# Kernel tuning notes

Measured on AMD Instinct MI355X. Metric: run time of the kernel, lower is better.

The kernel has to match this reference:

```python
import jax, jax.numpy as jnp
import numpy as np

N_NODES = 150000
N_EDGES = 4800000
IN_DIM, HID_DIM, OUT_DIM = 1433, 16, 7


def setup_inputs() -> dict:
    key = jax.random.key(0)
    ks = jax.random.split(key, 8)
    features = jax.random.normal(ks[0], (N_NODES, IN_DIM), dtype=jnp.float32)
    edge_src = jax.random.randint(ks[1], (N_EDGES,), 0, N_NODES, dtype=jnp.int32)
    edge_dst = jax.random.randint(ks[2], (N_EDGES,), 0, N_NODES, dtype=jnp.int32)
    adj_vals = jax.random.uniform(ks[3], (N_EDGES,), dtype=jnp.float32)
    W1 = jax.random.normal(ks[4], (IN_DIM, HID_DIM), dtype=jnp.float32) * (1.0 / np.sqrt(IN_DIM))
    b1 = jnp.zeros((HID_DIM,), dtype=jnp.float32)
    W2 = jax.random.normal(ks[5], (HID_DIM, OUT_DIM), dtype=jnp.float32) * (1.0 / np.sqrt(HID_DIM))
    b2 = jnp.zeros((OUT_DIM,), dtype=jnp.float32)
    return {"features": features, "edge_src": edge_src, "edge_dst": edge_dst,
            "adj_vals": adj_vals, "W1": W1, "b1": b1, "W2": W2, "b2": b2}


def _gcn_layer(x, edge_src, edge_dst, adj_vals, W, b):
    # h = A_hat @ (x @ W) + b ; dense transform first since in_dim >= out_dim
    xw = x @ W                                   # [N, d_out]
    msg = adj_vals[:, None] * xw[edge_src]       # [E, d_out] gather
    agg = jax.ops.segment_sum(msg, edge_dst, num_segments=x.shape[0])  # scatter-add
    return agg + b


def reference(features, edge_src, edge_dst, adj_vals, W1, b1, W2, b2):
    h1 = jax.nn.relu(_gcn_layer(features, edge_src, edge_dst, adj_vals, W1, b1))
    # dropout in original forward is a no-op (result discarded) -> omitted
    h2 = _gcn_layer(h1, edge_src, edge_dst, adj_vals, W2, b2)
    return jax.nn.log_softmax(h2, axis=1)
```

## Files before the change

### kernel.cpp

```cpp
#include <hip/hip_runtime.h>
#include <float.h>
#include <stdint.h>

#define IN_DIM 1433
#define HID 16
#define OUTD 7

#define KC 32
#define GROWS 64
#define NT 45
#define KLAST 25

#define AS1 __attribute__((address_space(1)))
#define AS3 __attribute__((address_space(3)))

__global__ __launch_bounds__(256, 4) void gemm1_kernel(
    const float* __restrict__ feat, const float* __restrict__ W1,
    float* __restrict__ xw1, int N)
{
    __shared__ float xs[3][GROWS * KC];
    const int t = threadIdx.x;
    const int lane = t & 63;
    const int w = t >> 6;
    const int row0 = blockIdx.x * GROWS;
    const long maxElem = (long)N * IN_DIM - 1;

    const int r  = t & 63;
    const int rb = r & 7;
    const int q4 = __builtin_amdgcn_readfirstlane(w) * 4;

    long ebase[8];
#pragma unroll
    for (int i = 0; i < 8; ++i) {
        const int ri = (i * 4 + w) * 2 + (lane >> 5);
        const int cs = lane & 31;
        const int gcol = (cs & 3) | (((cs >> 2) ^ (ri & 7)) << 2);
        ebase[i] = (long)(row0 + ri) * IN_DIM + gcol;
    }

    float acc[4] = {0.f, 0.f, 0.f, 0.f};

    auto stage = [&](int buf, int k0) {
#pragma unroll
        for (int i = 0; i < 8; ++i) {
            long elem = ebase[i] + k0;
            if (elem > maxElem) elem = maxElem;
            __builtin_amdgcn_global_load_lds(
                (const AS1 void*)(feat + elem),
                (AS3 void*)(&xs[buf][(i * 4 + w) * 64]), 4, 0, 0);
        }
    };

#define COMPUTE(buf, k0v, KMAX)                                              \
    {                                                                        \
        const float* xrow = &xs[buf][r * KC];                                \
        _Pragma("unroll")                                                    \
        for (int b = 0; b < ((KMAX) >> 2); ++b) {                            \
            const float4 xv = *(const float4*)&xrow[((b ^ rb) << 2)];        \
            const float* wk = W1 + (size_t)((k0v) + 4 * b) * HID + q4;       \
            const float4 w0 = *(const float4*)(wk);                          \
            const float4 w1 = *(const float4*)(wk + HID);                    \
            const float4 w2 = *(const float4*)(wk + 2 * HID);                \
            const float4 w3 = *(const float4*)(wk + 3 * HID);                \
            acc[0] += xv.x * w0.x; acc[1] += xv.x * w0.y;                    \
            acc[2] += xv.x * w0.z; acc[3] += xv.x * w0.w;                    \
            acc[0] += xv.y * w1.x; acc[1] += xv.y * w1.y;                    \
            acc[2] += xv.y * w1.z; acc[3] += xv.y * w1.w;                    \
            acc[0] += xv.z * w2.x; acc[1] += xv.z * w2.y;                    \
            acc[2] += xv.z * w2.z; acc[3] += xv.z * w2.w;                    \
            acc[0] += xv.w * w3.x; acc[1] += xv.w * w3.y;                    \
            acc[2] += xv.w * w3.z; acc[3] += xv.w * w3.w;                    \
        }                                                                    \
        if ((KMAX) & 3) {                     \
            const int b = (KMAX) >> 2;                                       \
            const float4 xv = *(const float4*)&xrow[((b ^ rb) << 2)];        \
            const float* wk = W1 + (size_t)((k0v) + 4 * b) * HID + q4;       \
            const float4 w0 = *(const float4*)(wk);                          \
            acc[0] += xv.x * w0.x; acc[1] += xv.x * w0.y;                    \
            acc[2] += xv.x * w0.z; acc[3] += xv.x * w0.w;                    \
        }                                                                    \
    }

#define WAITBAR(Nimm)                                                        \
    asm volatile("s_waitcnt vmcnt(" #Nimm ")" ::: "memory");                 \
    __builtin_amdgcn_sched_barrier(0);                                       \
    __builtin_amdgcn_s_barrier();                                            \
    __builtin_amdgcn_sched_barrier(0);

    stage(0, 0);
    stage(1, KC);
    for (int g = 0; g < 13; ++g) {
        const int k0 = g * (3 * KC);
        WAITBAR(8); stage(2, k0 + 2 * KC); COMPUTE(0, k0, KC);
        WAITBAR(8); stage(0, k0 + 3 * KC); COMPUTE(1, k0 + KC, KC);
        WAITBAR(8); stage(1, k0 + 4 * KC); COMPUTE(2, k0 + 2 * KC, KC);
    }
    WAITBAR(8); stage(2, 41 * KC); COMPUTE(0, 39 * KC, KC);
    WAITBAR(8); stage(0, 42 * KC); COMPUTE(1, 40 * KC, KC);
    WAITBAR(8); stage(1, 43 * KC); COMPUTE(2, 41 * KC, KC);
    WAITBAR(8); stage(2, 44 * KC); COMPUTE(0, 42 * KC, KC);
    WAITBAR(8);                    COMPUTE(1, 43 * KC, KC);
    WAITBAR(0);                    COMPUTE(2, 44 * KC, KLAST);
#undef COMPUTE
#undef WAITBAR

    const int grow = row0 + r;
    if (grow < N)
        *(float4*)(xw1 + (size_t)grow * HID + q4) =
            make_float4(acc[0], acc[1], acc[2], acc[3]);
}

__global__ __launch_bounds__(256) void hist_kernel(
    const int* __restrict__ dst, int* __restrict__ cnt, int E)
{
    const int e = blockIdx.x * 256 + threadIdx.x;
    if (e < E) atomicAdd(&cnt[dst[e]], 1);
}

__global__ __launch_bounds__(256) void scan1_kernel(
    const int* __restrict__ cnt, int* __restrict__ offs,
    int* __restrict__ bsum, int N)
{
    __shared__ int lds[256];
    const int t = threadIdx.x, b = blockIdx.x;
    const int base = b * 1024 + t * 4;
    int c0 = 0, c1 = 0, c2 = 0, c3 = 0;
    if (base + 0 < N) c0 = cnt[base + 0];
    if (base + 1 < N) c1 = cnt[base + 1];
    if (base + 2 < N) c2 = cnt[base + 2];
    if (base + 3 < N) c3 = cnt[base + 3];
    const int s = c0 + c1 + c2 + c3;
    lds[t] = s;
    __syncthreads();
    for (int off = 1; off < 256; off <<= 1) {
        int v = (t >= off) ? lds[t - off] : 0;
        __syncthreads();
        lds[t] += v;
        __syncthreads();
    }
    const int excl = lds[t] - s;
    if (t == 255) bsum[b] = lds[255];
    int run = excl;
    if (base + 0 < N) { offs[base + 0] = run; run += c0; }
    if (base + 1 < N) { offs[base + 1] = run; run += c1; }
    if (base + 2 < N) { offs[base + 2] = run; run += c2; }
    if (base + 3 < N) { offs[base + 3] = run; run += c3; }
}

__global__ __launch_bounds__(256) void scan2_kernel(
    const int* __restrict__ bsum, int* __restrict__ bbase, int NB)
{
    __shared__ int lds[256];
    const int t = threadIdx.x;
    const int v = (t < NB) ? bsum[t] : 0;
    lds[t] = v;
    __syncthreads();
    for (int off = 1; off < 256; off <<= 1) {
        int u = (t >= off) ? lds[t - off] : 0;
        __syncthreads();
        lds[t] += u;
        __syncthreads();
    }
    bbase[t] = lds[t] - v;
}

__global__ __launch_bounds__(256) void scan3_kernel(
    int* __restrict__ offs, int* __restrict__ cursor,
    const int* __restrict__ bbase, int N, int E)
{
    const int t = threadIdx.x, b = blockIdx.x;
    const int add = bbase[b];
    const int base = b * 1024 + t * 4;
#pragma unroll
    for (int i = 0; i < 4; ++i) {
        const int idx = base + i;
        if (idx < N) {
            const int v = offs[idx] + add;
            offs[idx] = v;
            cursor[idx] = v;
        }
    }
    if (b == 0 && t == 0) offs[N] = E;
}

__global__ __launch_bounds__(256) void fill_kernel(
    const int* __restrict__ src, const int* __restrict__ dst,
    const float* __restrict__ a, int* __restrict__ cursor,
    uint2* __restrict__ pairs, int E)
{
    const int e = blockIdx.x * 256 + threadIdx.x;
    if (e >= E) return;
    const int d = dst[e];
    const int pos = atomicAdd(&cursor[d], 1);
    pairs[pos] = make_uint2((unsigned)src[e], __float_as_uint(a[e]));
}

__global__ __launch_bounds__(256) void gather1_kernel(
    const uint2* __restrict__ pairs, const int* __restrict__ offs,
    const float* __restrict__ xw1, const float* __restrict__ b1,
    const float* __restrict__ W2, float* __restrict__ xw2, int N)
{
    __shared__ float w2s[HID * OUTD];
    const int t = threadIdx.x;
    if (t < HID * OUTD) w2s[t] = W2[t];
    __syncthreads();
    const int lane = t & 63;
    const int r = blockIdx.x * 4 + (t >> 6);
    if (r >= N) return;
    const int g = lane >> 2;
    const int c = lane & 3;
    const int start = offs[r], end = offs[r + 1];
    float4 acc = make_float4(0.f, 0.f, 0.f, 0.f);
    int e = start + g;
    for (; e + 16 < end; e += 32) {
        const uint2 p0 = pairs[e];
        const uint2 p1 = pairs[e + 16];
        const float4 v0 = *(const float4*)(xw1 + (size_t)p0.x * HID + c * 4);
        const float4 v1 = *(const float4*)(xw1 + (size_t)p1.x * HID + c * 4);
        const float a0 = __uint_as_float(p0.y);
        const float a1 = __uint_as_float(p1.y);
        acc.x += a0 * v0.x + a1 * v1.x;
        acc.y += a0 * v0.y + a1 * v1.y;
        acc.z += a0 * v0.z + a1 * v1.z;
        acc.w += a0 * v0.w + a1 * v1.w;
    }
    if (e < end) {
        const uint2 p0 = pairs[e];
        const float4 v0 = *(const float4*)(xw1 + (size_t)p0.x * HID + c * 4);
        const float a0 = __uint_as_float(p0.y);
        acc.x += a0 * v0.x; acc.y += a0 * v0.y;
        acc.z += a0 * v0.z; acc.w += a0 * v0.w;
    }
#pragma unroll
    for (int m = 4; m < 64; m <<= 1) {
        acc.x += __shfl_xor(acc.x, m);
        acc.y += __shfl_xor(acc.y, m);
        acc.z += __shfl_xor(acc.z, m);
        acc.w += __shfl_xor(acc.w, m);
    }
    const float4 b1v = ((const float4*)b1)[c];
    float4 hv;
    hv.x = fmaxf(acc.x + b1v.x, 0.f);
    hv.y = fmaxf(acc.y + b1v.y, 0.f);
    hv.z = fmaxf(acc.z + b1v.z, 0.f);
    hv.w = fmaxf(acc.w + b1v.w, 0.f);
    float hh[16];
#pragma unroll
    for (int cc = 0; cc < 4; ++cc) {
        hh[cc * 4 + 0] = __shfl(hv.x, cc);
        hh[cc * 4 + 1] = __shfl(hv.y, cc);
        hh[cc * 4 + 2] = __shfl(hv.z, cc);
        hh[cc * 4 + 3] = __shfl(hv.w, cc);
    }
    const int col = (lane & 7) < OUTD ? (lane & 7) : 0;
    float sacc = 0.f;
#pragma unroll
    for (int j = 0; j < HID; ++j) sacc += hh[j] * w2s[j * OUTD + col];
    if (lane < 8) xw2[(size_t)r * 8 + lane] = (lane < OUTD) ? sacc : 0.f;
}

__global__ __launch_bounds__(256) void gather2_kernel(
    const uint2* __restrict__ pairs, const int* __restrict__ offs,
    const float* __restrict__ xw2, const float* __restrict__ b2,
    float* __restrict__ out, int N)
{
    const int t = threadIdx.x;
    const int lane = t & 63;
    const int r = blockIdx.x * 4 + (t >> 6);
    if (r >= N) return;
    const int g = lane >> 1;
    const int c = lane & 1;
    const int start = offs[r], end = offs[r + 1];
    float4 acc = make_float4(0.f, 0.f, 0.f, 0.f);
    for (int e = start + g; e < end; e += 32) {
        const uint2 p = pairs[e];
        const float4 v = *(const float4*)(xw2 + (size_t)p.x * 8 + c * 4);
        const float a = __uint_as_float(p.y);
        acc.x += a * v.x; acc.y += a * v.y;
        acc.z += a * v.z; acc.w += a * v.w;
    }
#pragma unroll
    for (int m = 2; m < 64; m <<= 1) {
        acc.x += __shfl_xor(acc.x, m);
        acc.y += __shfl_xor(acc.y, m);
        acc.z += __shfl_xor(acc.z, m);
        acc.w += __shfl_xor(acc.w, m);
    }
    float4 x;
    if (c == 0) {
        const float4 b2v = *(const float4*)b2;
        x.x = acc.x + b2v.x; x.y = acc.y + b2v.y;
        x.z = acc.z + b2v.z; x.w = acc.w + b2v.w;
    } else {
        x.x = acc.x + b2[4]; x.y = acc.y + b2[5];
        x.z = acc.z + b2[6]; x.w = -FLT_MAX;
    }
    float mymax = fmaxf(fmaxf(x.x, x.y), x.z);
    if (c == 0) mymax = fmaxf(mymax, x.w);
    const float m = fmaxf(mymax, __shfl_xor(mymax, 1));
    float es = expf(x.x - m) + expf(x.y - m) + expf(x.z - m);
    if (c == 0) es += expf(x.w - m);
    const float s = es + __shfl_xor(es, 1);
    const float lg = logf(s);
    float* op = out + (size_t)r * OUTD;
    if (c == 0) {
        op[0] = x.x - m - lg; op[1] = x.y - m - lg;
        op[2] = x.z - m - lg; op[3] = x.w - m - lg;
    } else {
        op[4] = x.x - m - lg; op[5] = x.y - m - lg;
        op[6] = x.z - m - lg;
    }
}

extern "C" void kernel_launch(void* const* d_in, const int* in_sizes, int n_in,
                              void* d_out, int out_size, void* d_ws, size_t ws_size,
                              hipStream_t stream)
{
    const float* feat  = (const float*)d_in[0];
    const int*   esrc  = (const int*)d_in[1];
    const int*   edst  = (const int*)d_in[2];
    const float* avals = (const float*)d_in[3];
    const float* W1    = (const float*)d_in[4];
    const float* b1    = (const float*)d_in[5];
    const float* W2    = (const float*)d_in[6];
    const float* b2    = (const float*)d_in[7];
    float* out = (float*)d_out;

    const int N = in_sizes[0] / IN_DIM;
    const int E = in_sizes[1];
    const int NB = (N + 1023) / 1024;

    char* p = (char*)d_ws;
    float* xw1   = (float*)p; p += (size_t)N * HID * sizeof(float);
    float* xw2   = (float*)p; p += (size_t)N * 8 * sizeof(float);
    int*   cnt   = (int*)p;   p += (size_t)N * sizeof(int);
    int*   offs  = (int*)p;   p += (size_t)(N + 1) * sizeof(int);
    int*   cursor= (int*)p;   p += (size_t)N * sizeof(int);
    int*   bsum  = (int*)p;   p += 256 * sizeof(int);
    int*   bbase = (int*)p;   p += 256 * sizeof(int);
    p = (char*)(((uintptr_t)p + 15) & ~(uintptr_t)15);
    uint2* pairs = (uint2*)p;

    hipMemsetAsync(cnt, 0, (size_t)N * sizeof(int), stream);

    gemm1_kernel<<<(N + GROWS - 1) / GROWS, 256, 0, stream>>>(feat, W1, xw1, N);

    hist_kernel<<<(E + 255) / 256, 256, 0, stream>>>(edst, cnt, E);
    scan1_kernel<<<NB, 256, 0, stream>>>(cnt, offs, bsum, N);
    scan2_kernel<<<1, 256, 0, stream>>>(bsum, bbase, NB);
    scan3_kernel<<<NB, 256, 0, stream>>>(offs, cursor, bbase, N, E);
    fill_kernel<<<(E + 255) / 256, 256, 0, stream>>>(esrc, edst, avals, cursor, pairs, E);

    gather1_kernel<<<(N + 3) / 4, 256, 0, stream>>>(pairs, offs, xw1, b1, W2, xw2, N);
    gather2_kernel<<<(N + 3) / 4, 256, 0, stream>>>(pairs, offs, xw2, b2, out, N);
}
```

Baseline: 1.181 ms.

## Make GEMM1 wave-independent: each wave owns 64 rows and all 16 outputs

Restructures the feature GEMM so that each wavefront stages its own 64 rows into private LDS buffers and computes all 16 hidden outputs per row. Before, four waves shared the tile and each computed a 4-column slice. The triple-buffered pipeline with block-wide s_barrier becomes double buffering with only vmcnt waits, which removes inter-wave synchronisation. The cost is 16 accumulators per thread, 32 async loads per stage per wave and smaller 128-thread blocks, which raises register pressure and changes occupancy.

```diff
diff --git a/kernel.cpp b/kernel.cpp
--- a/kernel.cpp
+++ b/kernel.cpp
@@ -7,107 +7,117 @@
 #define OUTD 7
 
 #define KC 32
-#define GROWS 64
 #define NT 45
-#define KLAST 25
 
 #define AS1 __attribute__((address_space(1)))
 #define AS3 __attribute__((address_space(3)))
 
-__global__ __launch_bounds__(256, 4) void gemm1_kernel(
+__global__ __launch_bounds__(128, 2) void gemm1_kernel(
     const float* __restrict__ feat, const float* __restrict__ W1,
     float* __restrict__ xw1, int N)
 {
-    __shared__ float xs[3][GROWS * KC];
+    __shared__ float xs[2][2][64 * KC];
     const int t = threadIdx.x;
     const int lane = t & 63;
     const int w = t >> 6;
-    const int row0 = blockIdx.x * GROWS;
+    const int row0 = blockIdx.x * 128 + w * 64;
+    const int l5 = lane >> 5;
+    const int cs = lane & 31;
     const long maxElem = (long)N * IN_DIM - 1;
 
-    const int r  = t & 63;
-    const int rb = r & 7;
-    const int q4 = __builtin_amdgcn_readfirstlane(w) * 4;
-
-    long ebase[8];
-#pragma unroll
-    for (int i = 0; i < 8; ++i) {
-        const int ri = (i * 4 + w) * 2 + (lane >> 5);
-        const int cs = lane & 31;
-        const int gcol = (cs & 3) | (((cs >> 2) ^ (ri & 7)) << 2);
-        ebase[i] = (long)(row0 + ri) * IN_DIM + gcol;
-    }
-
-    float acc[4] = {0.f, 0.f, 0.f, 0.f};
+    int co[4];
+#pragma unroll
+    for (int m = 0; m < 4; ++m)
+        co[m] = (cs & 3) | (((cs >> 2) ^ ((2 * m + l5) & 7)) << 2);
+
+    const long A = (long)(row0 + l5) * IN_DIM;
 
     auto stage = [&](int buf, int k0) {
 #pragma unroll
-        for (int i = 0; i < 8; ++i) {
-            long elem = ebase[i] + k0;
+        for (int i = 0; i < 32; ++i) {
+            long elem = A + (long)(2 * i) * IN_DIM + k0 + co[i & 3];
             if (elem > maxElem) elem = maxElem;
             __builtin_amdgcn_global_load_lds(
                 (const AS1 void*)(feat + elem),
-                (AS3 void*)(&xs[buf][(i * 4 + w) * 64]), 4, 0, 0);
+                (AS3 void*)(&xs[w][buf][(2 * i) * KC]), 4, 0, 0);
         }
     };
 
-#define COMPUTE(buf, k0v, KMAX)                                              \
+    const int r  = lane;
+    const int rb = r & 7;
+    float acc[16];
+#pragma unroll
+    for (int j = 0; j < 16; ++j) acc[j] = 0.f;
+
+#define COMPUTE(buf, k0v, NB4, TAIL)                                         \
     {                                                                        \
-        const float* xrow = &xs[buf][r * KC];                                \
+        const float* xrow = &xs[w][buf][r * KC];                             \
         _Pragma("unroll")                                                    \
-        for (int b = 0; b < ((KMAX) >> 2); ++b) {                            \
+        for (int b = 0; b < (NB4); ++b) {                                    \
             const float4 xv = *(const float4*)&xrow[((b ^ rb) << 2)];        \
-            const float* wk = W1 + (size_t)((k0v) + 4 * b) * HID + q4;       \
-            const float4 w0 = *(const float4*)(wk);                          \
-            const float4 w1 = *(const float4*)(wk + HID);                    \
-            const float4 w2 = *(const float4*)(wk + 2 * HID);                \
-            const float4 w3 = *(const float4*)(wk + 3 * HID);                \
-            acc[0] += xv.x * w0.x; acc[1] += xv.x * w0.y;                    \
-            acc[2] += xv.x * w0.z; acc[3] += xv.x * w0.w;                    \
-            acc[0] += xv.y * w1.x; acc[1] += xv.y * w1.y;                    \
-            acc[2] += xv.y * w1.z; acc[3] += xv.y * w1.w;                    \
-            acc[0] += xv.z * w2.x; acc[1] += xv.z * w2.y;                    \
-            acc[2] += xv.z * w2.z; acc[3] += xv.z * w2.w;                    \
-            acc[0] += xv.w * w3.x; acc[1] += xv.w * w3.y;                    \
-            acc[2] += xv.w * w3.z; acc[3] += xv.w * w3.w;                    \
+            const float* wk = W1 + (size_t)((k0v) + 4 * b) * HID;            \
+            _Pragma("unroll")                                                \
+            for (int e = 0; e < 4; ++e) {                                    \
+                const float xe = ((const float*)&xv)[e];                     \
+                const float4 wA = *(const float4*)(wk + e * HID);            \
+                const float4 wB = *(const float4*)(wk + e * HID + 4);        \
+                const float4 wC = *(const float4*)(wk + e * HID + 8);        \
+                const float4 wD = *(const float4*)(wk + e * HID + 12);       \
+                acc[0]  += xe * wA.x; acc[1]  += xe * wA.y;                  \
+                acc[2]  += xe * wA.z; acc[3]  += xe * wA.w;                  \
+                acc[4]  += xe * wB.x; acc[5]  += xe * wB.y;                  \
+                acc[6]  += xe * wB.z; acc[7]  += xe * wB.w;                  \
+                acc[8]  += xe * wC.x; acc[9]  += xe * wC.y;                  \
+                acc[10] += xe * wC.z; acc[11] += xe * wC.w;                  \
+                acc[12] += xe * wD.x; acc[13] += xe * wD.y;                  \
+                acc[14] += xe * wD.z; acc[15] += xe * wD.w;                  \
+            }                                                                \
         }                                                                    \
-        if ((KMAX) & 3) {                     \
-            const int b = (KMAX) >> 2;                                       \
-            const float4 xv = *(const float4*)&xrow[((b ^ rb) << 2)];        \
-            const float* wk = W1 + (size_t)((k0v) + 4 * b) * HID + q4;       \
-            const float4 w0 = *(const float4*)(wk);                          \
-            acc[0] += xv.x * w0.x; acc[1] += xv.x * w0.y;                    \
-            acc[2] += xv.x * w0.z; acc[3] += xv.x * w0.w;                    \
+        if (TAIL) {                      \
+            const float4 xv = *(const float4*)&xrow[((6 ^ rb) << 2)];        \
+            const float xe = xv.x;                                           \
+            const float* wk = W1 + (size_t)((k0v) + 24) * HID;               \
+            const float4 wA = *(const float4*)(wk);                          \
+            const float4 wB = *(const float4*)(wk + 4);                      \
+            const float4 wC = *(const float4*)(wk + 8);                      \
+            const float4 wD = *(const float4*)(wk + 12);                     \
+            acc[0]  += xe * wA.x; acc[1]  += xe * wA.y;                      \
+            acc[2]  += xe * wA.z; acc[3]  += xe * wA.w;                      \
+            acc[4]  += xe * wB.x; acc[5]  += xe * wB.y;                      \
+            acc[6]  += xe * wB.z; acc[7]  += xe * wB.w;                      \
+            acc[8]  += xe * wC.x; acc[9]  += xe * wC.y;                      \
+            acc[10] += xe * wC.z; acc[11] += xe * wC.w;                      \
+            acc[12] += xe * wD.x; acc[13] += xe * wD.y;                      \
+            acc[14] += xe * wD.z; acc[15] += xe * wD.w;                      \
         }                                                                    \
     }
 
-#define WAITBAR(Nimm)                                                        \
+#define WAITVM(Nimm)                                                         \
     asm volatile("s_waitcnt vmcnt(" #Nimm ")" ::: "memory");                 \
-    __builtin_amdgcn_sched_barrier(0);                                       \
-    __builtin_amdgcn_s_barrier();                                            \
     __builtin_amdgcn_sched_barrier(0);
 
     stage(0, 0);
-    stage(1, KC);
-    for (int g = 0; g < 13; ++g) {
-        const int k0 = g * (3 * KC);
-        WAITBAR(8); stage(2, k0 + 2 * KC); COMPUTE(0, k0, KC);
-        WAITBAR(8); stage(0, k0 + 3 * KC); COMPUTE(1, k0 + KC, KC);
-        WAITBAR(8); stage(1, k0 + 4 * KC); COMPUTE(2, k0 + 2 * KC, KC);
-    }
-    WAITBAR(8); stage(2, 41 * KC); COMPUTE(0, 39 * KC, KC);
-    WAITBAR(8); stage(0, 42 * KC); COMPUTE(1, 40 * KC, KC);
-    WAITBAR(8); stage(1, 43 * KC); COMPUTE(2, 41 * KC, KC);
-    WAITBAR(8); stage(2, 44 * KC); COMPUTE(0, 42 * KC, KC);
-    WAITBAR(8);                    COMPUTE(1, 43 * KC, KC);
-    WAITBAR(0);                    COMPUTE(2, 44 * KC, KLAST);
+    for (int g = 0; g < 22; ++g) {
+        stage(1, (2 * g + 1) * KC);
+        WAITVM(32);
+        COMPUTE(0, 2 * g * KC, 8, false);
+        stage(0, (2 * g + 2) * KC);
+        WAITVM(32);
+        COMPUTE(1, (2 * g + 1) * KC, 8, false);
+    }
+    WAITVM(0);
+    COMPUTE(0, 44 * KC, 6, true);
 #undef COMPUTE
-#undef WAITBAR
+#undef WAITVM
 
     const int grow = row0 + r;
-    if (grow < N)
-        *(float4*)(xw1 + (size_t)grow * HID + q4) =
-            make_float4(acc[0], acc[1], acc[2], acc[3]);
+    if (grow < N) {
+        float4* o = (float4*)(xw1 + (size_t)grow * HID);
+        o[0] = make_float4(acc[0],  acc[1],  acc[2],  acc[3]);
+        o[1] = make_float4(acc[4],  acc[5],  acc[6],  acc[7]);
+        o[2] = make_float4(acc[8],  acc[9],  acc[10], acc[11]);
+        o[3] = make_float4(acc[12], acc[13], acc[14], acc[15]);
+    }
 }
 
 __global__ __launch_bounds__(256) void hist_kernel(
@@ -343,7 +353,7 @@
 
     hipMemsetAsync(cnt, 0, (size_t)N * sizeof(int), stream);
 
-    gemm1_kernel<<<(N + GROWS - 1) / GROWS, 256, 0, stream>>>(feat, W1, xw1, N);
+    gemm1_kernel<<<(N + 127) / 128, 128, 0, stream>>>(feat, W1, xw1, N);
 
     hist_kernel<<<(E + 255) / 256, 256, 0, stream>>>(edst, cnt, E);
     scan1_kernel<<<NB, 256, 0, stream>>>(cnt, offs, bsum, N);
```

After: 1.117 ms. 5.4% less time.
